# Kernel optimization log

Hardware: AMD Instinct MI355X
Metric: run time of the kernel (lower is better)

## Reference

```python
import jax, jax.numpy as jnp
import numpy as np

N_NODES = 50000
N_EDGES = 640000
HIDDEN = 128
LN_EPS = 1e-5


def setup_inputs() -> dict:
    key = jax.random.key(0)
    k_h, k_e, k_w1, k_w2 = jax.random.split(key, 4)
    s = 1.0 / np.sqrt(HIDDEN)
    return {
        "h": jax.random.normal(k_h, (N_NODES, HIDDEN), dtype=jnp.float32),
        "edge_index": jax.random.randint(k_e, (2, N_EDGES), 0, N_NODES, dtype=jnp.int32),
        "W1": jax.random.normal(k_w1, (HIDDEN, HIDDEN), dtype=jnp.float32) * s,
        "b1": jnp.zeros((HIDDEN,), dtype=jnp.float32),
        "W2": jax.random.normal(k_w2, (HIDDEN, HIDDEN), dtype=jnp.float32) * s,
        "b2": jnp.zeros((HIDDEN,), dtype=jnp.float32),
        "eps": jnp.zeros((), dtype=jnp.float32),  # GINConv train_eps init
        "gamma": jnp.ones((HIDDEN,), dtype=jnp.float32),
        "beta": jnp.zeros((HIDDEN,), dtype=jnp.float32),
    }


def reference(h, edge_index, W1, b1, W2, b2, eps, gamma, beta):
    src, dst = edge_index[0], edge_index[1]
    # GIN aggregation: sum of neighbor features scattered to destination nodes
    agg = jax.ops.segment_sum(h[src], dst, num_segments=h.shape[0])  # (N, D)
    z = (1.0 + eps) * h + agg
    # 2-layer MLP: Linear -> ReLU -> Linear (torch Linear: x @ W.T + b)
    z = jax.nn.relu(z @ W1.T + b1)
    h_conv = z @ W2.T + b2
    # residual + LayerNorm + ReLU (dropout is identity in eval mode)
    h_res = h_conv + h
    mu = jnp.mean(h_res, axis=-1, keepdims=True)
    var = jnp.var(h_res, axis=-1, keepdims=True)
    h_norm = (h_res - mu) * jax.lax.rsqrt(var + LN_EPS) * gamma + beta
    return jax.nn.relu(h_norm)
```

## Files before the change

### kernel.cpp

```cpp
#include <hip/hip_runtime.h>

#define HID 128
#define LN_EPS 1e-5f
#define LDSW 136

typedef __attribute__((ext_vector_type(8))) short bf16x8;
typedef __attribute__((ext_vector_type(4))) float f32x4;

static __device__ __forceinline__ unsigned short f2bf(float f) {
  unsigned int x = __float_as_uint(f);
  x += 0x7fffu + ((x >> 16) & 1u);
  return (unsigned short)(x >> 16);
}
static __device__ __forceinline__ float bflo(unsigned int u) { return __uint_as_float(u << 16); }
static __device__ __forceinline__ float bfhi(unsigned int u) { return __uint_as_float(u & 0xffff0000u); }

__global__ __launch_bounds__(256) void k_cvt_rank(const float* __restrict__ h,
                                                  const float* __restrict__ w1,
                                                  const float* __restrict__ w2,
                                                  uint2* __restrict__ hb,
                                                  uint2* __restrict__ w1b,
                                                  uint2* __restrict__ w2b,
                                                  int nh4, int nw4,
                                                  const int* __restrict__ ei,
                                                  int* __restrict__ counts,
                                                  int* __restrict__ rank,
                                                  int nE, int EB) {
  if ((int)blockIdx.x < EB) {
    const int e = blockIdx.x * 256 + threadIdx.x;
    if (e < nE) {
      const int d = ei[nE + e];
      rank[e] = atomicAdd(&counts[d], 1);
    }
    return;
  }
  const int total = nh4 + 2 * nw4;
  const int stride = (gridDim.x - EB) * 256;
  for (int i = (blockIdx.x - EB) * 256 + threadIdx.x; i < total; i += stride) {
    const float* src;
    uint2* dst;
    int off;
    if (i < nh4) { src = h; dst = hb; off = i; }
    else if (i < nh4 + nw4) { src = w1; dst = w1b; off = i - nh4; }
    else { src = w2; dst = w2b; off = i - nh4 - nw4; }
    const float4 v = reinterpret_cast<const float4*>(src)[off];
    uint2 p;
    p.x = (unsigned)f2bf(v.x) | ((unsigned)f2bf(v.y) << 16);
    p.y = (unsigned)f2bf(v.z) | ((unsigned)f2bf(v.w) << 16);
    dst[off] = p;
  }
}

__global__ __launch_bounds__(256) void k_scan1(const int* __restrict__ counts,
                                               int* __restrict__ offsets,
                                               int* __restrict__ bsum, int n) {
  __shared__ int sm[256];
  const int t = threadIdx.x;
  const int i = blockIdx.x * 256 + t;
  const int v = (i < n) ? counts[i] : 0;
  int incl = v;
  sm[t] = incl;
  __syncthreads();
#pragma unroll
  for (int off = 1; off < 256; off <<= 1) {
    const int other = (t >= off) ? sm[t - off] : 0;
    __syncthreads();
    incl += other;
    sm[t] = incl;
    __syncthreads();
  }
  if (i < n) offsets[i] = incl - v;
  if (t == 255) bsum[blockIdx.x] = incl;
}

__global__ __launch_bounds__(256) void k_scan2(const int* __restrict__ bsum,
                                               int* __restrict__ ebase,
                                               int* __restrict__ offsets,
                                               int nb, int n) {
  __shared__ int sm[256];
  const int t = threadIdx.x;
  const int v = (t < nb) ? bsum[t] : 0;
  int incl = v;
  sm[t] = incl;
  __syncthreads();
#pragma unroll
  for (int off = 1; off < 256; off <<= 1) {
    const int other = (t >= off) ? sm[t - off] : 0;
    __syncthreads();
    incl += other;
    sm[t] = incl;
    __syncthreads();
  }
  if (t < nb) ebase[t] = incl - v;
  if (t == 255) offsets[n] = incl;
}

__global__ __launch_bounds__(256) void k_scan3(int* __restrict__ offsets,
                                               const int* __restrict__ ebase, int n) {
  const int i = blockIdx.x * 256 + threadIdx.x;
  if (i >= n) return;
  offsets[i] += ebase[blockIdx.x];
}

__global__ __launch_bounds__(256) void k_scat(const int* __restrict__ ei,
                                              const int* __restrict__ rank,
                                              const int* __restrict__ offsets,
                                              int* __restrict__ esrc, int nE) {
  const int e = blockIdx.x * 256 + threadIdx.x;
  if (e >= nE) return;
  const int d = ei[nE + e];
  esrc[offsets[d] + rank[e]] = ei[e];
}

__global__ __launch_bounds__(256) void k_gather(const unsigned short* __restrict__ hbf,
                                                const int* __restrict__ offsets,
                                                const int* __restrict__ esrc,
                                                const float* __restrict__ eps,
                                                unsigned short* __restrict__ zbf, int nNodes) {
  const int gid = blockIdx.x * 256 + threadIdx.x;
  const int node = gid >> 5;
  if (node >= nNodes) return;
  const int col4 = (threadIdx.x & 31) * 4;
  const float c = 1.0f + eps[0];

  const uint2 hv = *reinterpret_cast<const uint2*>(hbf + (size_t)node * HID + col4);
  float a0 = c * bflo(hv.x), a1 = c * bfhi(hv.x);
  float a2 = c * bflo(hv.y), a3 = c * bfhi(hv.y);

  const int beg = offsets[node], end = offsets[node + 1];
  int e = beg;
  for (; e + 1 < end; e += 2) {
    const int s0 = esrc[e], s1 = esrc[e + 1];
    const uint2 v0 = *reinterpret_cast<const uint2*>(hbf + (size_t)s0 * HID + col4);
    const uint2 v1 = *reinterpret_cast<const uint2*>(hbf + (size_t)s1 * HID + col4);
    a0 += bflo(v0.x) + bflo(v1.x);
    a1 += bfhi(v0.x) + bfhi(v1.x);
    a2 += bflo(v0.y) + bflo(v1.y);
    a3 += bfhi(v0.y) + bfhi(v1.y);
  }
  if (e < end) {
    const uint2 v0 = *reinterpret_cast<const uint2*>(hbf + (size_t)esrc[e] * HID + col4);
    a0 += bflo(v0.x); a1 += bfhi(v0.x); a2 += bflo(v0.y); a3 += bfhi(v0.y);
  }
  uint2 o;
  o.x = (unsigned)f2bf(a0) | ((unsigned)f2bf(a1) << 16);
  o.y = (unsigned)f2bf(a2) | ((unsigned)f2bf(a3) << 16);
  *reinterpret_cast<uint2*>(zbf + (size_t)node * HID + col4) = o;
}

__global__ __launch_bounds__(256) void k_mmf(const unsigned short* __restrict__ zbf,
                                             const unsigned short* __restrict__ w1,
                                             const unsigned short* __restrict__ w2,
                                             const float* __restrict__ b1,
                                             const float* __restrict__ b2,
                                             const float* __restrict__ h,
                                             const float* __restrict__ gamma,
                                             const float* __restrict__ beta,
                                             float* __restrict__ out, int nTiles) {
  __shared__ unsigned short yt[16][LDSW];
  __shared__ float lnp[16][4][2];
  const int wave = threadIdx.x >> 6;
  const int l = threadIdx.x & 63;
  const int mtile = blockIdx.x;
  if (mtile >= nTiles) return;
  const int row0 = mtile * 16;
  const int lr = l & 15;
  const int lq = l >> 4;

  bf16x8 a[4];
#pragma unroll
  for (int ks = 0; ks < 4; ++ks)
    a[ks] = *reinterpret_cast<const bf16x8*>(zbf + (size_t)(row0 + lr) * HID + ks * 32 + lq * 8);

  f32x4 acc[2];
#pragma unroll
  for (int j = 0; j < 2; ++j) acc[j] = (f32x4){0.f, 0.f, 0.f, 0.f};
#pragma unroll
  for (int j = 0; j < 2; ++j) {
    const int nt = wave * 2 + j;
    const unsigned short* wb = w1 + (size_t)(nt * 16 + lr) * HID + lq * 8;
#pragma unroll
    for (int ks = 0; ks < 4; ++ks) {
      const bf16x8 b = *reinterpret_cast<const bf16x8*>(wb + ks * 32);
      acc[j] = __builtin_amdgcn_mfma_f32_16x16x32_bf16(a[ks], b, acc[j], 0, 0, 0);
    }
  }

#pragma unroll
  for (int j = 0; j < 2; ++j) {
    const int cc = (wave * 2 + j) * 16 + lr;
    const float bs = b1[cc];
#pragma unroll
    for (int r = 0; r < 4; ++r)
      yt[lq * 4 + r][cc] = f2bf(fmaxf(acc[j][r] + bs, 0.f));
  }
  __syncthreads();

  bf16x8 a2[4];
#pragma unroll
  for (int ks = 0; ks < 4; ++ks)
    a2[ks] = *reinterpret_cast<const bf16x8*>(&yt[lr][ks * 32 + lq * 8]);

#pragma unroll
  for (int j = 0; j < 2; ++j) acc[j] = (f32x4){0.f, 0.f, 0.f, 0.f};
#pragma unroll
  for (int j = 0; j < 2; ++j) {
    const int nt = wave * 2 + j;
    const unsigned short* wb = w2 + (size_t)(nt * 16 + lr) * HID + lq * 8;
#pragma unroll
    for (int ks = 0; ks < 4; ++ks) {
      const bf16x8 b = *reinterpret_cast<const bf16x8*>(wb + ks * 32);
      acc[j] = __builtin_amdgcn_mfma_f32_16x16x32_bf16(a2[ks], b, acc[j], 0, 0, 0);
    }
  }

#pragma unroll
  for (int j = 0; j < 2; ++j) {
    const int cc = (wave * 2 + j) * 16 + lr;
    const float bs = b2[cc];
#pragma unroll
    for (int r = 0; r < 4; ++r) {
      const int row = row0 + lq * 4 + r;
      acc[j][r] += bs + h[(size_t)row * HID + cc];
    }
  }

#pragma unroll
  for (int r = 0; r < 4; ++r) {
    float s = acc[0][r] + acc[1][r];
    float ss = acc[0][r] * acc[0][r] + acc[1][r] * acc[1][r];
#pragma unroll
    for (int m = 1; m < 16; m <<= 1) {
      s += __shfl_xor(s, m, 64);
      ss += __shfl_xor(ss, m, 64);
    }
    if (lr == 0) {
      lnp[lq * 4 + r][wave][0] = s;
      lnp[lq * 4 + r][wave][1] = ss;
    }
  }
  __syncthreads();

  float mu_[4], rstd_[4];
#pragma unroll
  for (int r = 0; r < 4; ++r) {
    const int rt = lq * 4 + r;
    float s = 0.f, ss = 0.f;
#pragma unroll
    for (int w = 0; w < 4; ++w) {
      const float2 p = *reinterpret_cast<const float2*>(&lnp[rt][w][0]);
      s += p.x;
      ss += p.y;
    }
    const float mu = s * (1.f / 128.f);
    const float var = ss * (1.f / 128.f) - mu * mu;
    mu_[r] = mu;
    rstd_[r] = rsqrtf(var + LN_EPS);
  }
#pragma unroll
  for (int j = 0; j < 2; ++j) {
    const int cc = (wave * 2 + j) * 16 + lr;
    const float g = gamma[cc], be = beta[cc];
#pragma unroll
    for (int r = 0; r < 4; ++r) {
      const int row = row0 + lq * 4 + r;
      const float o = (acc[j][r] - mu_[r]) * rstd_[r] * g + be;
      out[(size_t)row * HID + cc] = fmaxf(o, 0.f);
    }
  }
}

extern "C" void kernel_launch(void* const* d_in, const int* in_sizes, int n_in,
                              void* d_out, int out_size, void* d_ws, size_t ws_size,
                              hipStream_t stream) {
  const float* h     = (const float*)d_in[0];
  const int*   ei    = (const int*)d_in[1];
  const float* W1    = (const float*)d_in[2];
  const float* b1    = (const float*)d_in[3];
  const float* W2    = (const float*)d_in[4];
  const float* b2    = (const float*)d_in[5];
  const float* eps   = (const float*)d_in[6];
  const float* gamma = (const float*)d_in[7];
  const float* beta  = (const float*)d_in[8];

  const int nNodes = in_sizes[0] / HID;
  const int nE     = in_sizes[1] / 2;
  const int nb     = (nNodes + 255) / 256;
  const int nh4    = nNodes * HID / 4;
  const int nw4    = HID * HID / 4;

  int* counts  = (int*)d_ws;
  int* offsets = counts + nNodes;
  int* bsum    = offsets + nNodes + 1;
  int* ebase   = bsum + nb;
  int* rank    = counts + 100800;
  int* esrc    = rank + nE;
  unsigned short* hbf  = (unsigned short*)(esrc + nE);
  unsigned short* zbf  = hbf + (size_t)nNodes * HID;
  unsigned short* w1bf = zbf + (size_t)nNodes * HID;
  unsigned short* w2bf = w1bf + HID * HID;

  hipMemsetAsync(counts, 0, (size_t)nNodes * sizeof(int), stream);

  const int EB = (nE + 255) / 256;
  k_cvt_rank<<<EB + 2048, 256, 0, stream>>>(h, W1, W2, (uint2*)hbf, (uint2*)w1bf, (uint2*)w2bf,
                                            nh4, nw4, ei, counts, rank, nE, EB);
  k_scan1<<<nb, 256, 0, stream>>>(counts, offsets, bsum, nNodes);
  k_scan2<<<1, 256, 0, stream>>>(bsum, ebase, offsets, nb, nNodes);
  k_scan3<<<nb, 256, 0, stream>>>(offsets, ebase, nNodes);
  k_scat<<<EB, 256, 0, stream>>>(ei, rank, offsets, esrc, nE);

  k_gather<<<(nNodes * 32 + 255) / 256, 256, 0, stream>>>(hbf, offsets, esrc, eps, zbf, nNodes);

  const int nTiles = nNodes / 16;
  k_mmf<<<nTiles, 256, 0, stream>>>(zbf, w1bf, w2bf, b1, b2, h, gamma, beta,
                                    (float*)d_out, nTiles);
}
```

Before: 212.7 us.

## Fuse three-pass scan into single-pass lookback scan, unroll gather, hoist epilogue loads

Replaces the three scan kernels with one decoupled-lookback scan that chains block prefixes through flag-tagged 64-bit status words, removing two kernel launches and the intermediate block-sum buffer. The gather loop now issues four neighbor loads per iteration instead of two, giving more memory-level parallelism. The fused MLP kernel loads the residual h, biases, gamma and beta at the start so their latency overlaps the matrix multiplies. The lookback spins on earlier blocks, which assumes those blocks get scheduled, and the memset grows to clear the status words.

Measured after the change: 203.1 us. -4.5%, faster.

```diff
diff --git a/kernel.cpp b/kernel.cpp
--- a/kernel.cpp
+++ b/kernel.cpp
@@ -51,12 +51,15 @@
   }
 }
 
-__global__ __launch_bounds__(256) void k_scan1(const int* __restrict__ counts,
-                                               int* __restrict__ offsets,
-                                               int* __restrict__ bsum, int n) {
+__global__ __launch_bounds__(256) void k_scanLB(const int* __restrict__ counts,
+                                                int* __restrict__ offsets,
+                                                unsigned long long* st, int n, int nb) {
   __shared__ int sm[256];
+  __shared__ float baseSh_f;
+  __shared__ int baseSh;
   const int t = threadIdx.x;
-  const int i = blockIdx.x * 256 + t;
+  const int bid = blockIdx.x;
+  const int i = bid * 256 + t;
   const int v = (i < n) ? counts[i] : 0;
   int incl = v;
   sm[t] = incl;
@@ -69,37 +72,35 @@
     sm[t] = incl;
     __syncthreads();
   }
-  if (i < n) offsets[i] = incl - v;
-  if (t == 255) bsum[blockIdx.x] = incl;
-}
-
-__global__ __launch_bounds__(256) void k_scan2(const int* __restrict__ bsum,
-                                               int* __restrict__ ebase,
-                                               int* __restrict__ offsets,
-                                               int nb, int n) {
-  __shared__ int sm[256];
-  const int t = threadIdx.x;
-  const int v = (t < nb) ? bsum[t] : 0;
-  int incl = v;
-  sm[t] = incl;
+  const int total = sm[255];
+
+  if (bid == 0) {
+    if (t == 0) {
+      atomicExch(&st[0], (2ULL << 32) | (unsigned)total);
+      baseSh = 0;
+    }
+  } else {
+    if (t == 255)
+      atomicExch(&st[bid], (1ULL << 32) | (unsigned)total);
+    if (t == 0) {
+      long long base = 0;
+      int j = bid - 1;
+      while (j >= 0) {
+        unsigned long long p;
+        while (((p = atomicAdd(&st[j], 0ULL)) >> 32) == 0) __builtin_amdgcn_s_sleep(1);
+        base += (unsigned)p;
+        if ((p >> 32) == 2ULL) break;
+        --j;
+      }
+      atomicExch(&st[bid], (2ULL << 32) | (unsigned)(base + total));
+      baseSh = (int)base;
+    }
+  }
   __syncthreads();
-#pragma unroll
-  for (int off = 1; off < 256; off <<= 1) {
-    const int other = (t >= off) ? sm[t - off] : 0;
-    __syncthreads();
-    incl += other;
-    sm[t] = incl;
-    __syncthreads();
-  }
-  if (t < nb) ebase[t] = incl - v;
-  if (t == 255) offsets[n] = incl;
-}
-
-__global__ __launch_bounds__(256) void k_scan3(int* __restrict__ offsets,
-                                               const int* __restrict__ ebase, int n) {
-  const int i = blockIdx.x * 256 + threadIdx.x;
-  if (i >= n) return;
-  offsets[i] += ebase[blockIdx.x];
+  const int base = baseSh;
+  if (i < n) offsets[i] = base + incl - v;
+  if (bid == nb - 1 && t == 255) offsets[n] = base + total;
+  (void)baseSh_f;
 }
 
 __global__ __launch_bounds__(256) void k_scat(const int* __restrict__ ei,
@@ -129,16 +130,18 @@
 
   const int beg = offsets[node], end = offsets[node + 1];
   int e = beg;
-  for (; e + 1 < end; e += 2) {
-    const int s0 = esrc[e], s1 = esrc[e + 1];
+  for (; e + 3 < end; e += 4) {
+    const int s0 = esrc[e], s1 = esrc[e + 1], s2 = esrc[e + 2], s3 = esrc[e + 3];
     const uint2 v0 = *reinterpret_cast<const uint2*>(hbf + (size_t)s0 * HID + col4);
     const uint2 v1 = *reinterpret_cast<const uint2*>(hbf + (size_t)s1 * HID + col4);
-    a0 += bflo(v0.x) + bflo(v1.x);
-    a1 += bfhi(v0.x) + bfhi(v1.x);
-    a2 += bflo(v0.y) + bflo(v1.y);
-    a3 += bfhi(v0.y) + bfhi(v1.y);
-  }
-  if (e < end) {
+    const uint2 v2 = *reinterpret_cast<const uint2*>(hbf + (size_t)s2 * HID + col4);
+    const uint2 v3 = *reinterpret_cast<const uint2*>(hbf + (size_t)s3 * HID + col4);
+    a0 += (bflo(v0.x) + bflo(v1.x)) + (bflo(v2.x) + bflo(v3.x));
+    a1 += (bfhi(v0.x) + bfhi(v1.x)) + (bfhi(v2.x) + bfhi(v3.x));
+    a2 += (bflo(v0.y) + bflo(v1.y)) + (bflo(v2.y) + bflo(v3.y));
+    a3 += (bfhi(v0.y) + bfhi(v1.y)) + (bfhi(v2.y) + bfhi(v3.y));
+  }
+  for (; e < end; ++e) {
     const uint2 v0 = *reinterpret_cast<const uint2*>(hbf + (size_t)esrc[e] * HID + col4);
     a0 += bflo(v0.x); a1 += bfhi(v0.x); a2 += bflo(v0.y); a3 += bfhi(v0.y);
   }
@@ -161,12 +164,25 @@
   __shared__ float lnp[16][4][2];
   const int wave = threadIdx.x >> 6;
   const int l = threadIdx.x & 63;
-  const int mtile = blockIdx.x;
-  if (mtile >= nTiles) return;
-  const int row0 = mtile * 16;
+  const int row0 = blockIdx.x * 16;
   const int lr = l & 15;
   const int lq = l >> 4;
 
+  float hres[2][4];
+#pragma unroll
+  for (int j = 0; j < 2; ++j) {
+    const int cc = (wave * 2 + j) * 16 + lr;
+#pragma unroll
+    for (int r = 0; r < 4; ++r)
+      hres[j][r] = h[(size_t)(row0 + lq * 4 + r) * HID + cc];
+  }
+  float bs1[2], bs2[2], gg[2], bb[2];
+#pragma unroll
+  for (int j = 0; j < 2; ++j) {
+    const int cc = (wave * 2 + j) * 16 + lr;
+    bs1[j] = b1[cc]; bs2[j] = b2[cc]; gg[j] = gamma[cc]; bb[j] = beta[cc];
+  }
+
   bf16x8 a[4];
 #pragma unroll
   for (int ks = 0; ks < 4; ++ks)
@@ -177,8 +193,7 @@
   for (int j = 0; j < 2; ++j) acc[j] = (f32x4){0.f, 0.f, 0.f, 0.f};
 #pragma unroll
   for (int j = 0; j < 2; ++j) {
-    const int nt = wave * 2 + j;
-    const unsigned short* wb = w1 + (size_t)(nt * 16 + lr) * HID + lq * 8;
+    const unsigned short* wb = w1 + (size_t)((wave * 2 + j) * 16 + lr) * HID + lq * 8;
 #pragma unroll
     for (int ks = 0; ks < 4; ++ks) {
       const bf16x8 b = *reinterpret_cast<const bf16x8*>(wb + ks * 32);
@@ -189,10 +204,9 @@
 #pragma unroll
   for (int j = 0; j < 2; ++j) {
     const int cc = (wave * 2 + j) * 16 + lr;
-    const float bs = b1[cc];
 #pragma unroll
     for (int r = 0; r < 4; ++r)
-      yt[lq * 4 + r][cc] = f2bf(fmaxf(acc[j][r] + bs, 0.f));
+      yt[lq * 4 + r][cc] = f2bf(fmaxf(acc[j][r] + bs1[j], 0.f));
   }
   __syncthreads();
 
@@ -205,8 +219,7 @@
   for (int j = 0; j < 2; ++j) acc[j] = (f32x4){0.f, 0.f, 0.f, 0.f};
 #pragma unroll
   for (int j = 0; j < 2; ++j) {
-    const int nt = wave * 2 + j;
-    const unsigned short* wb = w2 + (size_t)(nt * 16 + lr) * HID + lq * 8;
+    const unsigned short* wb = w2 + (size_t)((wave * 2 + j) * 16 + lr) * HID + lq * 8;
 #pragma unroll
     for (int ks = 0; ks < 4; ++ks) {
       const bf16x8 b = *reinterpret_cast<const bf16x8*>(wb + ks * 32);
@@ -215,15 +228,10 @@
   }
 
 #pragma unroll
-  for (int j = 0; j < 2; ++j) {
-    const int cc = (wave * 2 + j) * 16 + lr;
-    const float bs = b2[cc];
-#pragma unroll
-    for (int r = 0; r < 4; ++r) {
-      const int row = row0 + lq * 4 + r;
-      acc[j][r] += bs + h[(size_t)row * HID + cc];
-    }
-  }
+  for (int j = 0; j < 2; ++j)
+#pragma unroll
+    for (int r = 0; r < 4; ++r)
+      acc[j][r] += bs2[j] + hres[j][r];
 
 #pragma unroll
   for (int r = 0; r < 4; ++r) {
@@ -260,14 +268,14 @@
 #pragma unroll
   for (int j = 0; j < 2; ++j) {
     const int cc = (wave * 2 + j) * 16 + lr;
-    const float g = gamma[cc], be = beta[cc];
 #pragma unroll
     for (int r = 0; r < 4; ++r) {
       const int row = row0 + lq * 4 + r;
-      const float o = (acc[j][r] - mu_[r]) * rstd_[r] * g + be;
+      const float o = (acc[j][r] - mu_[r]) * rstd_[r] * gg[j] + bb[j];
       out[(size_t)row * HID + cc] = fmaxf(o, 0.f);
     }
   }
+  (void)nTiles;
 }
 
 extern "C" void kernel_launch(void* const* d_in, const int* in_sizes, int n_in,
@@ -291,8 +299,7 @@
 
   int* counts  = (int*)d_ws;
   int* offsets = counts + nNodes;
-  int* bsum    = offsets + nNodes + 1;
-  int* ebase   = bsum + nb;
+  unsigned long long* st = (unsigned long long*)(counts + 100002);
   int* rank    = counts + 100800;
   int* esrc    = rank + nE;
   unsigned short* hbf  = (unsigned short*)(esrc + nE);
@@ -300,14 +307,12 @@
   unsigned short* w1bf = zbf + (size_t)nNodes * HID;
   unsigned short* w2bf = w1bf + HID * HID;
 
-  hipMemsetAsync(counts, 0, (size_t)nNodes * sizeof(int), stream);
+  hipMemsetAsync(counts, 0, (size_t)(100002 + 2 * nb) * sizeof(int), stream);
 
   const int EB = (nE + 255) / 256;
   k_cvt_rank<<<EB + 2048, 256, 0, stream>>>(h, W1, W2, (uint2*)hbf, (uint2*)w1bf, (uint2*)w2bf,
                                             nh4, nw4, ei, counts, rank, nE, EB);
-  k_scan1<<<nb, 256, 0, stream>>>(counts, offsets, bsum, nNodes);
-  k_scan2<<<1, 256, 0, stream>>>(bsum, ebase, offsets, nb, nNodes);
-  k_scan3<<<nb, 256, 0, stream>>>(offsets, ebase, nNodes);
+  k_scanLB<<<nb, 256, 0, stream>>>(counts, offsets, st, nNodes, nb);
   k_scat<<<EB, 256, 0, stream>>>(ei, rank, offsets, esrc, nE);
 
   k_gather<<<(nNodes * 32 + 255) / 256, 256, 0, stream>>>(hbf, offsets, esrc, eps, zbf, nNodes);
```
